# Kernel optimization log

Hardware: AMD Instinct MI355X
Metric: run time of the kernel (lower is better)

Reference implementation:

```python
import jax, jax.numpy as jnp
import numpy as np

N = 100000
E = 1600000
IN_DIM = 128
HID = 16      # per-head dim
HEADS = 4
FEAT = HID * HEADS  # 64
OUT_DIM = 64
EPS = 0.5
LAYERS = 2


def setup_inputs() -> dict:
    key = jax.random.key(0)
    ks = jax.random.split(key, 8)
    return {
        "h": jax.random.normal(ks[0], (N, IN_DIM), dtype=jnp.float32),
        "src": jax.random.randint(ks[1], (E,), 0, N, dtype=jnp.int64),
        "dst": jax.random.randint(ks[2], (E,), 0, N, dtype=jnp.int64),
        "t1_W": jax.random.normal(ks[3], (IN_DIM, FEAT), dtype=jnp.float32) * 0.1,
        "t1_b": jnp.zeros((FEAT,), dtype=jnp.float32),
        "t2_W": jax.random.normal(ks[4], (FEAT, OUT_DIM), dtype=jnp.float32) * 0.1,
        "t2_b": jnp.zeros((OUT_DIM,), dtype=jnp.float32),
        "gate_W": jax.random.normal(ks[5], (LAYERS, 2 * HID, 1), dtype=jnp.float32) * 0.2,
        "gate_b": jnp.zeros((LAYERS, 1), dtype=jnp.float32),
    }


def reference(h, src, dst, t1_W, t1_b, t2_W, t2_b, gate_W, gate_b):
    # t1 + relu
    x = jax.nn.relu(h @ t1_W + t1_b)            # [N, FEAT]
    raw = x

    # symmetric degree norm: deg^-0.5 from in-degrees (clamped at 1)
    deg = jax.ops.segment_sum(jnp.ones((E,), x.dtype), dst, num_segments=N)
    norm = jnp.clip(deg, 1.0, None) ** -0.5     # [N]

    xh = x.reshape(N, HEADS, HID)
    edge_norm = norm[dst] * norm[src]           # [E]
    h1 = raw
    # NOTE: original forward never updates x inside the loop; each layer
    # consumes the same relu(t1(h)) and only the last layer's h0 survives.
    for l in range(LAYERS):
        hs = xh[src]                            # [E, H, D] gather src
        hd = xh[dst]                            # [E, H, D] gather dst
        hcat = jnp.concatenate([hd, hs], axis=-1)  # [E, H, 2D]
        s = jnp.tanh(hcat @ gate_W[l] + gate_b[l])[..., 0]  # [E, H]
        s = s * edge_norm[:, None]
        e_h = (hs * s[..., None]).reshape(E, FEAT)          # [E, FEAT]
        h0 = jax.ops.segment_sum(e_h, dst, num_segments=N)  # scatter-sum
        h1 = EPS * raw + h0

    return h1 @ t2_W + t2_b                      # [N, OUT_DIM]
```

## Files before the change

### kernel.cpp

```cpp
#include <hip/hip_runtime.h>
#include <hip/hip_fp16.h>
#include <math.h>

#define N_NODES 100000
#define E_EDGES 1600000
#define IN_DIM  128
#define FEAT    64
#define OUT_DIM 64
#define NBKT    391
#define CAP     6144
#define RNG     4096
#define NSCB    ((E_EDGES + RNG - 1) / RNG)
#define G1B     ((N_NODES + 255) / 256)

typedef float vfloat2 __attribute__((ext_vector_type(2)));

__global__ __launch_bounds__(256) void k_binscatter(
    const int* __restrict__ src, const int* __restrict__ dst,
    int* __restrict__ bucket_cursor, int* __restrict__ binned)
{
    __shared__ int hist[NBKT];
    __shared__ int baseS[NBKT];
    __shared__ int cursor[NBKT];
    __shared__ int gbase[NBKT];
    __shared__ int sA[512], sB[512];
    __shared__ int buf[RNG];
    __shared__ unsigned short bkt[RNG];

    const int tid  = threadIdx.x;
    const int e0   = blockIdx.x * RNG;
    const int ecnt = min(RNG, E_EDGES - e0);

    for (int i = tid; i < NBKT; i += 256) hist[i] = 0;
    __syncthreads();

    int dsave[16];
#pragma unroll
    for (int k = 0; k < 16; ++k) {
        int e = e0 + k * 256 + tid;
        int d = (e < E_EDGES) ? dst[e] : -1;
        dsave[k] = d;
        if (d >= 0) atomicAdd(&hist[d >> 8], 1);
    }
    __syncthreads();

    for (int i = tid; i < 512; i += 256) sA[i] = (i < NBKT) ? hist[i] : 0;
    __syncthreads();
    int* pa = sA; int* pb = sB;
    for (int off = 1; off < 512; off <<= 1) {
        for (int i = tid; i < 512; i += 256)
            pb[i] = pa[i] + ((i >= off) ? pa[i - off] : 0);
        __syncthreads();
        int* t = pa; pa = pb; pb = t;
    }
    for (int i = tid; i < NBKT; i += 256) {
        int ex = pa[i] - hist[i];
        baseS[i]  = ex;
        cursor[i] = ex;
    }
    __syncthreads();

#pragma unroll
    for (int k = 0; k < 16; ++k) {
        int d = dsave[k];
        if (d >= 0) {
            int e   = e0 + k * 256 + tid;
            int s   = src[e];
            int b   = d >> 8;
            int pos = atomicAdd(&cursor[b], 1);
            buf[pos] = ((d & 255) << 17) | s;
            bkt[pos] = (unsigned short)b;
        }
    }
    __syncthreads();

    for (int t = tid; t < NBKT; t += 256) {
        int cnt = hist[t];
        int g   = cnt ? atomicAdd(&bucket_cursor[t], cnt) : 0;
        gbase[t] = g - baseS[t];
    }
    __syncthreads();

    for (int i = tid; i < ecnt; i += 256) {
        int b   = bkt[i];
        int off = gbase[b] + i;
        if (off < CAP) binned[b * CAP + off] = buf[i];
    }
}

__global__ __launch_bounds__(256) void k_bucketfinal(
    const int* __restrict__ binned, const int* __restrict__ bucket_cursor,
    int* __restrict__ deg, int* __restrict__ rowptr, int* __restrict__ src_sorted)
{
    __shared__ int sA[512], sB[512];
    __shared__ int hist[256];
    __shared__ int scn[256];
    __shared__ int cur[256];
    const int b   = blockIdx.x;
    const int tid = threadIdx.x;

    for (int i = tid; i < 512; i += 256) sA[i] = (i < NBKT) ? bucket_cursor[i] : 0;
    __syncthreads();
    int* pa = sA; int* pb = sB;
    for (int off = 1; off < 512; off <<= 1) {
        for (int i = tid; i < 512; i += 256)
            pb[i] = pa[i] + ((i >= off) ? pa[i - off] : 0);
        __syncthreads();
        int* t = pa; pa = pb; pb = t;
    }
    const int cnt  = bucket_cursor[b];
    const int eb   = pa[b] - cnt;
    const int base = b * CAP;
    __syncthreads();

    hist[tid] = 0;
    __syncthreads();
    for (int i = tid; i < cnt; i += 256)
        atomicAdd(&hist[binned[base + i] >> 17], 1);
    __syncthreads();

    int v = hist[tid];
    scn[tid] = v;
    __syncthreads();
    for (int off = 1; off < 256; off <<= 1) {
        int add = (tid >= off) ? scn[tid - off] : 0;
        __syncthreads();
        scn[tid] += add;
        __syncthreads();
    }
    int ex = scn[tid] - v;
    cur[tid] = ex;
    int n = b * 256 + tid;
    if (n < N_NODES) {
        deg[n]    = v;
        rowptr[n] = eb + ex;
    }
    if (b == 0 && tid == 0) rowptr[N_NODES] = E_EDGES;
    __syncthreads();

    for (int i = tid; i < cnt; i += 256) {
        int p   = binned[base + i];
        int dl  = p >> 17;
        int pos = atomicAdd(&cur[dl], 1);
        src_sorted[eb + pos] = p & 0x1FFFF;
    }
}

__global__ __launch_bounds__(256, 3) void k_gemm1(
    const float* __restrict__ h, const float* __restrict__ W1,
    const float* __restrict__ b1, const int* __restrict__ deg,
    const float* __restrict__ gate_W,
    __half* __restrict__ xs2h, unsigned int* __restrict__ xq,
    float* __restrict__ aproj, float* __restrict__ bproj)
{
    __shared__ float Ws[IN_DIM * FEAT];
    __shared__ float hT[16 * 260];
    const int tid = threadIdx.x;
    const int r0  = blockIdx.x * 256;

    for (int i = tid; i < IN_DIM * FEAT / 4; i += 256)
        ((float4*)Ws)[i] = ((const float4*)W1)[i];

    const int rg = tid >> 2;
    const int cg = tid & 3;
    const int c0 = cg * 16;
    float acc[4][16];
#pragma unroll
    for (int i = 0; i < 4; ++i)
#pragma unroll
        for (int j = 0; j < 16; ++j) acc[i][j] = 0.f;

    const int  myrow = r0 + tid;
    const bool rok   = myrow < N_NODES;

    for (int kc = 0; kc < IN_DIM / 16; ++kc) {
        float4 f[4];
        if (rok) {
            const float4* hp = (const float4*)(h + (size_t)myrow * IN_DIM + kc * 16);
            f[0] = hp[0]; f[1] = hp[1]; f[2] = hp[2]; f[3] = hp[3];
        } else {
            f[0] = f[1] = f[2] = f[3] = make_float4(0.f, 0.f, 0.f, 0.f);
        }
        __syncthreads();
#pragma unroll
        for (int q = 0; q < 4; ++q) {
            hT[(q * 4 + 0) * 260 + tid] = f[q].x;
            hT[(q * 4 + 1) * 260 + tid] = f[q].y;
            hT[(q * 4 + 2) * 260 + tid] = f[q].z;
            hT[(q * 4 + 3) * 260 + tid] = f[q].w;
        }
        __syncthreads();
#pragma unroll
        for (int kk = 0; kk < 16; ++kk) {
            float4 a4 = *(const float4*)&hT[kk * 260 + rg * 4];
            const float* wrow = &Ws[(kc * 16 + kk) * FEAT + c0];
            float4 w0 = ((const float4*)wrow)[0];
            float4 w1 = ((const float4*)wrow)[1];
            float4 w2 = ((const float4*)wrow)[2];
            float4 w3 = ((const float4*)wrow)[3];
            const float a[4] = {a4.x, a4.y, a4.z, a4.w};
            const float w[16] = {w0.x, w0.y, w0.z, w0.w, w1.x, w1.y, w1.z, w1.w,
                                 w2.x, w2.y, w2.z, w2.w, w3.x, w3.y, w3.z, w3.w};
#pragma unroll
            for (int i = 0; i < 4; ++i)
#pragma unroll
                for (int j = 0; j < 16; ++j)
                    acc[i][j] = fmaf(a[i], w[j], acc[i][j]);
        }
    }

#pragma unroll
    for (int i = 0; i < 4; ++i) {
        int r = r0 + rg * 4 + i;
        if (r >= N_NODES) continue;
        float nr = rsqrtf(fmaxf((float)deg[r], 1.f));
        float xa = 0.f, xb = 0.f;
        alignas(16) __half hv[16];
        float vs[16];
#pragma unroll
        for (int j = 0; j < 16; ++j) {
            float v = acc[i][j] + b1[c0 + j];
            v = v > 0.f ? v : 0.f;
            xa = fmaf(v, gate_W[32 + j], xa);
            xb = fmaf(v, gate_W[48 + j], xb);
            float sv = v * nr;
            vs[j] = sv;
            hv[j] = __float2half(sv);
        }
        float4* xp = (float4*)(xs2h + (size_t)r * FEAT + c0);
        xp[0] = *(const float4*)&hv[0];
        xp[1] = *(const float4*)&hv[8];
        unsigned int u[4];
#pragma unroll
        for (int q = 0; q < 4; ++q) {
            unsigned int t = 0;
            t = __builtin_amdgcn_cvt_pk_fp8_f32(vs[q*4+0], vs[q*4+1], t, false);
            t = __builtin_amdgcn_cvt_pk_fp8_f32(vs[q*4+2], vs[q*4+3], t, true);
            u[q] = t;
        }
        ((uint4*)xq)[(size_t)r * 4 + cg] = make_uint4(u[0], u[1], u[2], u[3]);
        aproj[(size_t)r * 4 + cg] = xa;
        bproj[(size_t)r * 4 + cg] = xb;
    }
}

__global__ __launch_bounds__(256) void k_aggregate(
    const unsigned int* __restrict__ xq, const __half2* __restrict__ xs2h2,
    const float* __restrict__ aproj, const float* __restrict__ bproj,
    const int* __restrict__ rowptr, const int* __restrict__ src_sorted,
    const float* __restrict__ gate_b, float* __restrict__ v_out)
{
    const int tid    = threadIdx.x;
    const int lane   = tid & 63;
    const int q      = lane >> 4;
    const int l16    = lane & 15;
    const int head   = l16 >> 2;
    const int wave   = blockIdx.x * 4 + (tid >> 6);
    const int nwaves = gridDim.x * 4;
    const float gb   = gate_b[1];

    for (int n = wave; n < N_NODES; n += nwaves) {
        int beg = rowptr[n];
        int end = rowptr[n + 1];
        int cnt = end - beg;
        float a_d = aproj[(size_t)n * 4 + head] + gb;
        float4 acc = make_float4(0.f, 0.f, 0.f, 0.f);
        if (cnt > 0) {
            int  last = end - 1;
            int  j0   = beg + q;
            bool ok0  = j0 < end;
            int  s0   = src_sorted[ok0 ? j0 : last];
            unsigned int x0 = xq[(size_t)s0 * 16 + l16];
            float        b0 = bproj[(size_t)s0 * 4 + head];
            for (int j = beg; j < end; j += 4) {
                int  jn  = j + 4 + q;
                bool okn = jn < end;
                int  sn  = src_sorted[okn ? jn : last];
                unsigned int xn = xq[(size_t)sn * 16 + l16];
                float        bn = bproj[(size_t)sn * 4 + head];
                vfloat2 lo = __builtin_amdgcn_cvt_pk_f32_fp8(x0, false);
                vfloat2 hi = __builtin_amdgcn_cvt_pk_f32_fp8(x0, true);
                float e = __builtin_amdgcn_exp2f(2.8853900817779268f * (a_d + b0));
                float t = 1.f - 2.f * __builtin_amdgcn_rcpf(e + 1.f);
                t = ok0 ? t : 0.f;
                acc.x = fmaf(t, lo[0], acc.x);
                acc.y = fmaf(t, lo[1], acc.y);
                acc.z = fmaf(t, hi[0], acc.z);
                acc.w = fmaf(t, hi[1], acc.w);
                ok0 = okn; x0 = xn; b0 = bn;
            }
        }
        acc.x += __shfl_xor(acc.x, 16, 64);
        acc.y += __shfl_xor(acc.y, 16, 64);
        acc.z += __shfl_xor(acc.z, 16, 64);
        acc.w += __shfl_xor(acc.w, 16, 64);
        acc.x += __shfl_xor(acc.x, 32, 64);
        acc.y += __shfl_xor(acc.y, 32, 64);
        acc.z += __shfl_xor(acc.z, 32, 64);
        acc.w += __shfl_xor(acc.w, 32, 64);
        float dg = fmaxf((float)cnt, 1.f);
        float nd = rsqrtf(dg);
        float sd = dg * nd;
        if (q == 0) {
            __half2 ha = xs2h2[(size_t)n * 32 + l16 * 2];
            __half2 hb = xs2h2[(size_t)n * 32 + l16 * 2 + 1];
            float2 fa = __half22float2(ha);
            float2 fb = __half22float2(hb);
            float4 v;
            v.x = fmaf(0.5f * sd, fa.x, acc.x * nd);
            v.y = fmaf(0.5f * sd, fa.y, acc.y * nd);
            v.z = fmaf(0.5f * sd, fb.x, acc.z * nd);
            v.w = fmaf(0.5f * sd, fb.y, acc.w * nd);
            ((float4*)v_out)[(size_t)n * 16 + l16] = v;
        }
    }
}

__global__ __launch_bounds__(256, 3) void k_gemm2(
    float* __restrict__ v, const float* __restrict__ W2, const float* __restrict__ b2)
{
    __shared__ float Ws[FEAT * OUT_DIM];
    __shared__ float vT[16 * 260];
    const int tid = threadIdx.x;
    const int r0  = blockIdx.x * 256;

    for (int i = tid; i < FEAT * OUT_DIM / 4; i += 256)
        ((float4*)Ws)[i] = ((const float4*)W2)[i];

    const int rg = tid >> 2;
    const int cg = tid & 3;
    const int c0 = cg * 16;
    float acc[4][16];
#pragma unroll
    for (int i = 0; i < 4; ++i)
#pragma unroll
        for (int j = 0; j < 16; ++j) acc[i][j] = 0.f;

    const int  myrow = r0 + tid;
    const bool rok   = myrow < N_NODES;

    for (int kc = 0; kc < FEAT / 16; ++kc) {
        float4 f[4];
        if (rok) {
            const float4* vp = (const float4*)(v + (size_t)myrow * FEAT + kc * 16);
            f[0] = vp[0]; f[1] = vp[1]; f[2] = vp[2]; f[3] = vp[3];
        } else {
            f[0] = f[1] = f[2] = f[3] = make_float4(0.f, 0.f, 0.f, 0.f);
        }
        __syncthreads();
#pragma unroll
        for (int q = 0; q < 4; ++q) {
            vT[(q * 4 + 0) * 260 + tid] = f[q].x;
            vT[(q * 4 + 1) * 260 + tid] = f[q].y;
            vT[(q * 4 + 2) * 260 + tid] = f[q].z;
            vT[(q * 4 + 3) * 260 + tid] = f[q].w;
        }
        __syncthreads();
#pragma unroll
        for (int kk = 0; kk < 16; ++kk) {
            float4 a4 = *(const float4*)&vT[kk * 260 + rg * 4];
            const float* wrow = &Ws[(kc * 16 + kk) * OUT_DIM + c0];
            float4 w0 = ((const float4*)wrow)[0];
            float4 w1 = ((const float4*)wrow)[1];
            float4 w2 = ((const float4*)wrow)[2];
            float4 w3 = ((const float4*)wrow)[3];
            const float a[4] = {a4.x, a4.y, a4.z, a4.w};
            const float w[16] = {w0.x, w0.y, w0.z, w0.w, w1.x, w1.y, w1.z, w1.w,
                                 w2.x, w2.y, w2.z, w2.w, w3.x, w3.y, w3.z, w3.w};
#pragma unroll
            for (int i = 0; i < 4; ++i)
#pragma unroll
                for (int j = 0; j < 16; ++j)
                    acc[i][j] = fmaf(a[i], w[j], acc[i][j]);
        }
    }

#pragma unroll
    for (int i = 0; i < 4; ++i) {
        int r = r0 + rg * 4 + i;
        if (r >= N_NODES) continue;
        float* op = &v[(size_t)r * OUT_DIM + c0];
#pragma unroll
        for (int q = 0; q < 4; ++q) {
            float4 o = make_float4(acc[i][q*4]   + b2[c0 + q*4],
                                   acc[i][q*4+1] + b2[c0 + q*4 + 1],
                                   acc[i][q*4+2] + b2[c0 + q*4 + 2],
                                   acc[i][q*4+3] + b2[c0 + q*4 + 3]);
            ((float4*)op)[q] = o;
        }
    }
}

extern "C" void kernel_launch(void* const* d_in, const int* in_sizes, int n_in,
                              void* d_out, int out_size, void* d_ws, size_t ws_size,
                              hipStream_t stream)
{
    const float* h   = (const float*)d_in[0];
    const int*   src = (const int*)d_in[1];
    const int*   dst = (const int*)d_in[2];
    const float* W1  = (const float*)d_in[3];
    const float* b1  = (const float*)d_in[4];
    const float* W2  = (const float*)d_in[5];
    const float* b2  = (const float*)d_in[6];
    const float* gW  = (const float*)d_in[7];
    const float* gb  = (const float*)d_in[8];
    float* out = (float*)d_out;

    int* bucket_cursor = (int*)d_ws;
    int* binned        = bucket_cursor + NBKT;
    int* src_sorted    = binned + (size_t)NBKT * CAP;
    int* rowptr        = src_sorted + E_EDGES;
    int* deg           = rowptr + (N_NODES + 1);
    float* aproj       = (float*)(deg + N_NODES);
    float* bproj       = aproj + (size_t)N_NODES * 4;
    __half* xs2h       = (__half*)(bproj + (size_t)N_NODES * 4);
    unsigned int* xq   = (unsigned int*)(xs2h + (size_t)N_NODES * FEAT);

    hipMemsetAsync(bucket_cursor, 0, NBKT * sizeof(int), stream);

    k_binscatter <<<NSCB, 256, 0, stream>>>(src, dst, bucket_cursor, binned);
    k_bucketfinal<<<NBKT, 256, 0, stream>>>(binned, bucket_cursor, deg, rowptr, src_sorted);
    k_gemm1      <<<G1B, 256, 0, stream>>>(h, W1, b1, deg, gW, xs2h, xq, aproj, bproj);
    k_aggregate  <<<2048, 256, 0, stream>>>(xq, (const __half2*)xs2h, aproj, bproj,
                                            rowptr, src_sorted, gb, out);
    k_gemm2      <<<G1B, 256, 0, stream>>>(out, W2, b2);
}
```

Before: 268.7 us.

## Process 16 edges per wave iteration with uint4 fp8 loads and transpose-reduce

Changes the aggregation lane mapping from 4 edges per wave step (16 lanes each reading 4 fp8 bytes) to 16 edges per step, with each 4-lane group reading 16 bytes per lane as a uint4. Each lane now computes one head's gate and accumulates 16 features. The cross-lane reduction becomes a butterfly transpose-reduce, so the 64 results end up spread across 16 lanes. The goal is fewer loop iterations per node (average degree is 16), wider memory transactions, and deeper prefetch of source indices. The cost is more registers per lane and a heavier reduction phase.

```diff
diff --git a/kernel.cpp b/kernel.cpp
--- a/kernel.cpp
+++ b/kernel.cpp
@@ -245,73 +245,110 @@
 }
 
 __global__ __launch_bounds__(256) void k_aggregate(
-    const unsigned int* __restrict__ xq, const __half2* __restrict__ xs2h2,
+    const uint4* __restrict__ xq4, const __half2* __restrict__ xs2h2,
     const float* __restrict__ aproj, const float* __restrict__ bproj,
     const int* __restrict__ rowptr, const int* __restrict__ src_sorted,
     const float* __restrict__ gate_b, float* __restrict__ v_out)
 {
     const int tid    = threadIdx.x;
     const int lane   = tid & 63;
-    const int q      = lane >> 4;
-    const int l16    = lane & 15;
-    const int head   = l16 >> 2;
+    const int e      = lane >> 2;
+    const int l4     = lane & 3;
     const int wave   = blockIdx.x * 4 + (tid >> 6);
     const int nwaves = gridDim.x * 4;
     const float gb   = gate_b[1];
+    const float C    = 2.8853900817779268f;
 
     for (int n = wave; n < N_NODES; n += nwaves) {
-        int beg = rowptr[n];
-        int end = rowptr[n + 1];
-        int cnt = end - beg;
-        float a_d = aproj[(size_t)n * 4 + head] + gb;
-        float4 acc = make_float4(0.f, 0.f, 0.f, 0.f);
+        const int beg = rowptr[n];
+        const int end = rowptr[n + 1];
+        const int cnt = end - beg;
+        const float a_d = aproj[(size_t)n * 4 + l4] + gb;
+
+        float acc[16];
+#pragma unroll
+        for (int k = 0; k < 16; ++k) acc[k] = 0.f;
+
         if (cnt > 0) {
-            int  last = end - 1;
-            int  j0   = beg + q;
-            bool ok0  = j0 < end;
-            int  s0   = src_sorted[ok0 ? j0 : last];
-            unsigned int x0 = xq[(size_t)s0 * 16 + l16];
-            float        b0 = bproj[(size_t)s0 * 4 + head];
-            for (int j = beg; j < end; j += 4) {
-                int  jn  = j + 4 + q;
-                bool okn = jn < end;
-                int  sn  = src_sorted[okn ? jn : last];
-                unsigned int xn = xq[(size_t)sn * 16 + l16];
-                float        bn = bproj[(size_t)sn * 4 + head];
-                vfloat2 lo = __builtin_amdgcn_cvt_pk_f32_fp8(x0, false);
-                vfloat2 hi = __builtin_amdgcn_cvt_pk_f32_fp8(x0, true);
-                float e = __builtin_amdgcn_exp2f(2.8853900817779268f * (a_d + b0));
-                float t = 1.f - 2.f * __builtin_amdgcn_rcpf(e + 1.f);
+            const int last = end - 1;
+            int  j0  = beg + e;
+            bool ok0 = j0 < end;
+            int  s0  = src_sorted[ok0 ? j0 : last];
+            uint4 x0 = xq4[(size_t)s0 * 4 + l4];
+            float b0 = bproj[(size_t)s0 * 4 + l4];
+            int  j1  = j0 + 16;
+            bool ok1 = j1 < end;
+            int  s1  = src_sorted[ok1 ? j1 : last];
+
+            for (int j = beg; j < end; j += 16) {
+                const bool more = (j + 16) < end;
+                uint4 x1 = make_uint4(0u, 0u, 0u, 0u);
+                float b1 = 0.f;
+                int   s2 = s1;
+                bool  ok2 = false;
+                if (more) {
+                    x1 = xq4[(size_t)s1 * 4 + l4];
+                    b1 = bproj[(size_t)s1 * 4 + l4];
+                    int j2 = j + 32 + e;
+                    ok2 = j2 < end;
+                    s2 = src_sorted[ok2 ? j2 : last];
+                }
+                float ex = __builtin_amdgcn_exp2f(C * (a_d + b0));
+                float t  = 1.f - 2.f * __builtin_amdgcn_rcpf(ex + 1.f);
                 t = ok0 ? t : 0.f;
-                acc.x = fmaf(t, lo[0], acc.x);
-                acc.y = fmaf(t, lo[1], acc.y);
-                acc.z = fmaf(t, hi[0], acc.z);
-                acc.w = fmaf(t, hi[1], acc.w);
-                ok0 = okn; x0 = xn; b0 = bn;
+#pragma unroll
+                for (int w = 0; w < 4; ++w) {
+                    const unsigned int xw = ((const unsigned int*)&x0)[w];
+                    vfloat2 lo = __builtin_amdgcn_cvt_pk_f32_fp8(xw, false);
+                    vfloat2 hi = __builtin_amdgcn_cvt_pk_f32_fp8(xw, true);
+                    acc[w * 4 + 0] = fmaf(t, lo[0], acc[w * 4 + 0]);
+                    acc[w * 4 + 1] = fmaf(t, lo[1], acc[w * 4 + 1]);
+                    acc[w * 4 + 2] = fmaf(t, hi[0], acc[w * 4 + 2]);
+                    acc[w * 4 + 3] = fmaf(t, hi[1], acc[w * 4 + 3]);
+                }
+                if (more) {
+                    x0 = x1; b0 = b1; ok0 = ok1; ok1 = ok2; s1 = s2;
+                }
             }
         }
-        acc.x += __shfl_xor(acc.x, 16, 64);
-        acc.y += __shfl_xor(acc.y, 16, 64);
-        acc.z += __shfl_xor(acc.z, 16, 64);
-        acc.w += __shfl_xor(acc.w, 16, 64);
-        acc.x += __shfl_xor(acc.x, 32, 64);
-        acc.y += __shfl_xor(acc.y, 32, 64);
-        acc.z += __shfl_xor(acc.z, 32, 64);
-        acc.w += __shfl_xor(acc.w, 32, 64);
-        float dg = fmaxf((float)cnt, 1.f);
-        float nd = rsqrtf(dg);
-        float sd = dg * nd;
-        if (q == 0) {
-            __half2 ha = xs2h2[(size_t)n * 32 + l16 * 2];
-            __half2 hb = xs2h2[(size_t)n * 32 + l16 * 2 + 1];
-            float2 fa = __half22float2(ha);
-            float2 fb = __half22float2(hb);
+
+        const bool elo = (e & 1) == 0;
+        float r8[8];
+#pragma unroll
+        for (int i = 0; i < 8; ++i) {
+            float give = elo ? acc[8 + i] : acc[i];
+            float got  = __shfl_xor(give, 4, 64);
+            r8[i] = (elo ? acc[i] : acc[8 + i]) + got;
+        }
+        const bool e2lo = (e & 2) == 0;
+        float v4[4];
+#pragma unroll
+        for (int i = 0; i < 4; ++i) {
+            float give = e2lo ? r8[4 + i] : r8[i];
+            float got  = __shfl_xor(give, 8, 64);
+            v4[i] = (e2lo ? r8[i] : r8[4 + i]) + got;
+        }
+#pragma unroll
+        for (int i = 0; i < 4; ++i) v4[i] += __shfl_xor(v4[i], 16, 64);
+#pragma unroll
+        for (int i = 0; i < 4; ++i) v4[i] += __shfl_xor(v4[i], 32, 64);
+
+        const float dg = fmaxf((float)cnt, 1.f);
+        const float nd = rsqrtf(dg);
+        const float sd = dg * nd;
+
+        if (e < 4) {
+            const int q = ((e & 1) << 1) | ((e >> 1) & 1);
+            const int Q = l4 * 4 + q;
+            const __half2* hp = xs2h2 + (size_t)n * 32 + Q * 2;
+            float2 fa = __half22float2(hp[0]);
+            float2 fb = __half22float2(hp[1]);
             float4 v;
-            v.x = fmaf(0.5f * sd, fa.x, acc.x * nd);
-            v.y = fmaf(0.5f * sd, fa.y, acc.y * nd);
-            v.z = fmaf(0.5f * sd, fb.x, acc.z * nd);
-            v.w = fmaf(0.5f * sd, fb.y, acc.w * nd);
-            ((float4*)v_out)[(size_t)n * 16 + l16] = v;
+            v.x = fmaf(0.5f * sd, fa.x, v4[0] * nd);
+            v.y = fmaf(0.5f * sd, fa.y, v4[1] * nd);
+            v.z = fmaf(0.5f * sd, fb.x, v4[2] * nd);
+            v.w = fmaf(0.5f * sd, fb.y, v4[3] * nd);
+            ((float4*)v_out)[(size_t)n * 16 + Q] = v;
         }
     }
 }
@@ -421,7 +458,7 @@
     k_binscatter <<<NSCB, 256, 0, stream>>>(src, dst, bucket_cursor, binned);
     k_bucketfinal<<<NBKT, 256, 0, stream>>>(binned, bucket_cursor, deg, rowptr, src_sorted);
     k_gemm1      <<<G1B, 256, 0, stream>>>(h, W1, b1, deg, gW, xs2h, xq, aproj, bproj);
-    k_aggregate  <<<2048, 256, 0, stream>>>(xq, (const __half2*)xs2h, aproj, bproj,
-                                            rowptr, src_sorted, gb, out);
+    k_aggregate  <<<2048, 256, 0, stream>>>((const uint4*)xq, (const __half2*)xs2h,
+                                            aproj, bproj, rowptr, src_sorted, gb, out);
     k_gemm2      <<<G1B, 256, 0, stream>>>(out, W2, b2);
 }
```

After: 255.1 us. 5.0% less time.
